# Kernel optimization log

Hardware: AMD Instinct MI355X
Metric: run time of the kernel (lower is better)

Reference implementation:

```python
import jax, jax.numpy as jnp
import numpy as np

MAXU = 6          # init arg maxU
MAXV = 6          # init arg maxV (ratio=None)
TRUNC = 4         # cfg.TRUNCATED_SIZE; cfg.TRUNCATED=True, cfg.FLOW_REG_BY_MAX=True


def setup_inputs() -> dict:
    key = jax.random.key(0)
    B, H, W = 8, 128, 160
    U, V = 2 * MAXU + 1, 2 * MAXV + 1
    x = jax.random.normal(key, (B, 1, U, V, H, W), dtype=jnp.float32)
    return {"x": x}


def reference(x):
    # x: [B,1,U,V,H,W] cost volume
    x = x[:, 0]                                   # [B,U,V,H,W]
    b, u, v, h, w = x.shape

    # --- truncation mask (cfg.TRUNCATED) ---
    # argmax over flattened (u,v); scatter one-hot + MaxPool3d((2t+1,2t+1,1))
    # is equivalent to a +-t box around the per-pixel argmax location.
    idx = jnp.argmax(x.reshape(b, u * v, h, w), axis=1)   # [B,H,W] int
    ui = (idx // v)[:, None, None]                        # [B,1,1,H,W]
    vi = (idx % v)[:, None, None]
    ugrid = jnp.arange(u).reshape(1, u, 1, 1, 1)
    vgrid = jnp.arange(v).reshape(1, 1, v, 1, 1)
    mask = (jnp.abs(ugrid - ui) <= TRUNC) & (jnp.abs(vgrid - vi) <= TRUNC)
    xm = jnp.where(mask, x, -jnp.inf)

    # --- softmax over the U*V displacement hypotheses (FLOW_REG_BY_MAX) ---
    p = jax.nn.softmax(xm.reshape(b, u * v, h, w), axis=1).reshape(b, u, v, h, w)

    dispU = jnp.arange(-MAXU, MAXU + 1, dtype=x.dtype)    # [U]
    dispV = jnp.arange(-MAXV, MAXV + 1, dtype=x.dtype)    # [V]
    flowU = jnp.einsum('buvhw,u->bhw', p, dispU)
    flowV = jnp.einsum('buvhw,v->bhw', p, dispV)
    return jnp.stack((flowU, flowV), axis=1)              # [B,2,H,W]
```

## Files before the change

kernel.cpp:

```cpp
#include <hip/hip_runtime.h>
#include <math.h>

#define Bsz 8
#define Udim 13
#define Vdim 13
#define Hdim 128
#define Wdim 160
#define HW (Hdim * Wdim)
#define UV (Udim * Vdim)
#define TRUNC 4
#define NPIX (Bsz * HW)

__global__ __launch_bounds__(256, 2) void flow_regression_kernel(
    const float* __restrict__ x, float* __restrict__ out) {
    int p = blockIdx.x * 256 + threadIdx.x;
    int b  = p / HW;
    int hw = p - b * HW;

    const float* base = x + (size_t)b * UV * HW + hw;

    float vals[UV];
    #pragma unroll
    for (int i = 0; i < UV; ++i) {
        vals[i] = base[(size_t)i * HW];
    }

    float m = vals[0];
    int mi = 0;
    #pragma unroll
    for (int i = 1; i < UV; ++i) {
        if (vals[i] > m) { m = vals[i]; mi = i; }
    }
    int ui = mi / Vdim;
    int vi = mi - ui * Vdim;

    float sum = 0.f, wu = 0.f, wv = 0.f;
    #pragma unroll
    for (int u = 0; u < Udim; ++u) {
        bool uin = (u - ui <= TRUNC) && (ui - u <= TRUNC);
        float rsum = 0.f, rwv = 0.f;
        #pragma unroll
        for (int v = 0; v < Vdim; ++v) {
            float val = vals[u * Vdim + v];
            bool vin = (v - vi <= TRUNC) && (vi - v <= TRUNC);
            float e = vin ? __expf(val - m) : 0.f;
            rsum += e;
            rwv  += e * (float)(v - 6);
        }
        if (uin) {
            sum += rsum;
            wu  += rsum * (float)(u - 6);
            wv  += rwv;
        }
    }
    float inv = 1.0f / sum;
    float* ob = out + (size_t)b * 2 * HW + hw;
    ob[0]  = wu * inv;
    ob[HW] = wv * inv;
}

extern "C" void kernel_launch(void* const* d_in, const int* in_sizes, int n_in,
                              void* d_out, int out_size, void* d_ws, size_t ws_size,
                              hipStream_t stream) {
    const float* x = (const float*)d_in[0];
    float* out = (float*)d_out;
    flow_regression_kernel<<<NPIX / 256, 256, 0, stream>>>(x, out);
}
```

Measured before the change: 158.3 us.

## Split each pixel's displacement hypotheses across two half-waves with shuffle reductions

```diff
diff --git a/kernel.cpp b/kernel.cpp
--- a/kernel.cpp
+++ b/kernel.cpp
@@ -1,7 +1,6 @@
 #include <hip/hip_runtime.h>
 #include <math.h>
 
-#define Bsz 8
 #define Udim 13
 #define Vdim 13
 #define Hdim 128
@@ -9,54 +8,63 @@
 #define HW (Hdim * Wdim)
 #define UV (Udim * Vdim)
 #define TRUNC 4
-#define NPIX (Bsz * HW)
+#define NPIX (8 * HW)
+#define NPL 85
 
-__global__ __launch_bounds__(256, 2) void flow_regression_kernel(
+__global__ __launch_bounds__(256, 3) void flow_regression_kernel(
     const float* __restrict__ x, float* __restrict__ out) {
-    int p = blockIdx.x * 256 + threadIdx.x;
-    int b  = p / HW;
-    int hw = p - b * HW;
+    int t    = threadIdx.x;
+    int lane = t & 63;
+    int g    = lane >> 5;
+    int p32  = lane & 31;
+    int wave = t >> 6;
+    int pixel = blockIdx.x * 128 + wave * 32 + p32;
+    int b  = pixel / HW;
+    int hw = pixel - b * HW;
 
-    const float* base = x + (size_t)b * UV * HW + hw;
+    const float* base = x + (size_t)b * UV * HW + hw + (size_t)(g * NPL) * HW;
 
-    float vals[UV];
+    float vals[NPL];
     #pragma unroll
-    for (int i = 0; i < UV; ++i) {
-        vals[i] = base[(size_t)i * HW];
-    }
+    for (int i = 0; i < NPL - 1; ++i) vals[i] = base[(size_t)i * HW];
+    vals[NPL - 1] = (g == 0) ? base[(size_t)(NPL - 1) * HW] : -INFINITY;
 
     float m = vals[0];
     int mi = 0;
     #pragma unroll
-    for (int i = 1; i < UV; ++i) {
+    for (int i = 1; i < NPL; ++i)
         if (vals[i] > m) { m = vals[i]; mi = i; }
-    }
-    int ui = mi / Vdim;
+    mi += g * NPL;
+
+    float om = __shfl_xor(m, 32);
+    int   oi = __shfl_xor(mi, 32);
+    if (om > m || (om == m && oi < mi)) { m = om; mi = oi; }
+
+    int ui = (mi * 158) >> 11;
     int vi = mi - ui * Vdim;
 
-    float sum = 0.f, wu = 0.f, wv = 0.f;
+    float s = 0.f, su = 0.f, sv = 0.f;
+    int u = g ? 6 : 0, v = g ? 7 : 0;
     #pragma unroll
-    for (int u = 0; u < Udim; ++u) {
-        bool uin = (u - ui <= TRUNC) && (ui - u <= TRUNC);
-        float rsum = 0.f, rwv = 0.f;
-        #pragma unroll
-        for (int v = 0; v < Vdim; ++v) {
-            float val = vals[u * Vdim + v];
-            bool vin = (v - vi <= TRUNC) && (vi - v <= TRUNC);
-            float e = vin ? __expf(val - m) : 0.f;
-            rsum += e;
-            rwv  += e * (float)(v - 6);
-        }
-        if (uin) {
-            sum += rsum;
-            wu  += rsum * (float)(u - 6);
-            wv  += rwv;
-        }
+    for (int i = 0; i < NPL; ++i) {
+        bool in = (u - ui <= TRUNC) && (ui - u <= TRUNC) &&
+                  (v - vi <= TRUNC) && (vi - v <= TRUNC);
+        float e = in ? __expf(vals[i] - m) : 0.f;
+        s  += e;
+        su += e * (float)(u - 6);
+        sv += e * (float)(v - 6);
+        if (++v == Vdim) { v = 0; ++u; }
     }
-    float inv = 1.0f / sum;
-    float* ob = out + (size_t)b * 2 * HW + hw;
-    ob[0]  = wu * inv;
-    ob[HW] = wv * inv;
+    s  += __shfl_xor(s, 32);
+    su += __shfl_xor(su, 32);
+    sv += __shfl_xor(sv, 32);
+
+    if (g == 0) {
+        float inv = 1.0f / s;
+        float* ob = out + (size_t)b * 2 * HW + hw;
+        ob[0]  = su * inv;
+        ob[HW] = sv * inv;
+    }
 }
 
 extern "C" void kernel_launch(void* const* d_in, const int* in_sizes, int n_in,
@@ -64,5 +72,5 @@
                               hipStream_t stream) {
     const float* x = (const float*)d_in[0];
     float* out = (float*)d_out;
-    flow_regression_kernel<<<NPIX / 256, 256, 0, stream>>>(x, out);
+    flow_regression_kernel<<<NPIX / 128, 256, 0, stream>>>(x, out);
 }
```

New measurement: 162.8 us. 2.8% more time.
